# Performance work log

Measured on AMD Instinct MI355X. Metric: run time of the kernel, lower is better.

The kernel has to match this reference:

```python
import jax, jax.numpy as jnp
import numpy as np

D_MODEL = 1024
NHEAD = 16
D_K = D_MODEL // NHEAD


def setup_inputs() -> dict:
    key = jax.random.key(0)
    ks = jax.random.split(key, 12)
    B, L = 4, 2048
    s = 1.0 / np.sqrt(D_MODEL)
    inp = {
        "query": jax.random.normal(ks[0], (B, L, D_MODEL), jnp.float32),
        "key": jax.random.normal(ks[1], (B, L, D_MODEL), jnp.float32),
        "value": jax.random.normal(ks[2], (B, L, D_MODEL), jnp.float32),
        "Wq": jax.random.normal(ks[3], (D_MODEL, D_MODEL), jnp.float32) * s,
        "bq": jnp.zeros((D_MODEL,), jnp.float32),
        "Wk": jax.random.normal(ks[4], (D_MODEL, D_MODEL), jnp.float32) * s,
        "bk": jnp.zeros((D_MODEL,), jnp.float32),
        "Wv": jax.random.normal(ks[5], (D_MODEL, D_MODEL), jnp.float32) * s,
        "bv": jnp.zeros((D_MODEL,), jnp.float32),
        "Wo": jax.random.normal(ks[6], (D_MODEL, D_MODEL), jnp.float32) * s,
        "bo": jnp.zeros((D_MODEL,), jnp.float32),
    }
    return inp


def reference(query, key, value, Wq, bq, Wk, bk, Wv, bv, Wo, bo):
    B, Lq, _ = query.shape
    Lk = key.shape[1]
    # Linear projections, split into heads: [B, H, L, d_k]
    Q = (query @ Wq + bq).reshape(B, Lq, NHEAD, D_K).transpose(0, 2, 1, 3)
    K = (key @ Wk + bk).reshape(B, Lk, NHEAD, D_K).transpose(0, 2, 1, 3)
    V = (value @ Wv + bv).reshape(B, Lk, NHEAD, D_K).transpose(0, 2, 1, 3)
    scale = 1.0 / jnp.sqrt(jnp.asarray(D_K, Q.dtype))
    scores = jnp.einsum("bhqd,bhkd->bhqk", Q, K) * scale  # [B,H,Lq,Lk]
    attn = jax.nn.softmax(scores, axis=-1)
    context = jnp.einsum("bhqk,bhkd->bhqd", attn, V)
    context = context.transpose(0, 2, 1, 3).reshape(B, Lq, D_MODEL)
    return context @ Wo + bo
```

## Files before the change

kernel.cpp:

```cpp
#include <hip/hip_runtime.h>
#include <hip/hip_bf16.h>
#include <cstdint>
#include <cstddef>


typedef unsigned short u16;
typedef __bf16 bf8v __attribute__((ext_vector_type(8)));
typedef __bf16 bf4v __attribute__((ext_vector_type(4)));
typedef float f32x4 __attribute__((ext_vector_type(4)));

#define D_MODEL 1024
#define NHEAD   16
#define DK      64
#define BATCH   4
#define SEQ     2048
#define ROWS    (BATCH * SEQ)

__device__ __forceinline__ u16 f2b(float f) {
  union { float f; unsigned int i; } x; x.f = f;
  unsigned int r = x.i + 0x7fffu + ((x.i >> 16) & 1u);
  return (u16)(r >> 16);
}
__device__ __forceinline__ ushort4 pack4(float a, float b, float c, float d) {
  union { bf4v v; ushort4 u; } x;
  x.v[0] = (__bf16)a; x.v[1] = (__bf16)b; x.v[2] = (__bf16)c; x.v[3] = (__bf16)d;
  return x.u;
}
__device__ __forceinline__ void async16(const void* g, void* l) {
  __builtin_amdgcn_global_load_lds((const __attribute__((address_space(1))) void*)g,
                                   (__attribute__((address_space(3))) void*)l, 16, 0, 0);
}
#define MFMA16(a, b, c) __builtin_amdgcn_mfma_f32_16x16x32_bf16(a, b, c, 0, 0, 0)

__global__ void wtrans_cvt_kernel(const float* __restrict__ w0, const float* __restrict__ w1,
                                  const float* __restrict__ w2, const float* __restrict__ w3,
                                  u16* __restrict__ dst4) {
  __shared__ float t[32][33];
  const float* src = (blockIdx.z == 0) ? w0 : (blockIdx.z == 1) ? w1
                   : (blockIdx.z == 2) ? w2 : w3;
  u16* dst = dst4 + (size_t)blockIdx.z * D_MODEL * D_MODEL;
  const int c0 = blockIdx.x * 32, r0 = blockIdx.y * 32;
  for (int i = threadIdx.y; i < 32; i += 8)
    t[i][threadIdx.x] = src[(size_t)(r0 + i) * D_MODEL + c0 + threadIdx.x];
  __syncthreads();
  for (int i = threadIdx.y; i < 32; i += 8)
    dst[(size_t)(c0 + i) * D_MODEL + r0 + threadIdx.x] = f2b(t[threadIdx.x][i]);
}

__device__ __forceinline__ void gemm_epilogue(const f32x4 acc[4][4],
                                              const float* __restrict__ bias,
                                              void* __restrict__ out, int mode,
                                              float oscale, int m0, int n0,
                                              int wm, int wn, int quad, int l16) {
#pragma unroll
  for (int j = 0; j < 4; j++) {
    const int n = n0 + wn * 64 + j * 16 + l16;
    const float bv = bias[n];
#pragma unroll
    for (int i = 0; i < 4; i++) {
      const int gr0 = m0 + wm * 64 + i * 16 + quad * 4;
#pragma unroll
      for (int r = 0; r < 4; r++) {
        const int row = gr0 + r;
        const float val = (acc[i][j][r] + bv) * oscale;
        if (mode == 2) {
          ((float*)out)[(size_t)row * D_MODEL + n] = val;
        } else {
          const int b = row >> 11, l = row & 2047;
          const int h = n >> 6, d = n & 63;
          if (mode == 0)
            ((u16*)out)[(((size_t)(b * NHEAD + h) * SEQ + l) << 6) + d] = f2b(val);
          else
            ((u16*)out)[(((size_t)(b * NHEAD + h) * DK + d) << 11) + l] = f2b(val);
        }
      }
    }
  }
}

#define BM 128
#define BN 128
#define BK 32

__global__ __launch_bounds__(256) void gemm_qkv(const float* __restrict__ qa,
                                                const float* __restrict__ ka,
                                                const float* __restrict__ va,
                                                const u16* __restrict__ wt,
                                                const float* __restrict__ bq,
                                                const float* __restrict__ bk,
                                                const float* __restrict__ bv,
                                                u16* __restrict__ Qw, u16* __restrict__ Kw,
                                                u16* __restrict__ Vt, float qscale) {
  const int z = blockIdx.z;
  const float* A   = (z == 0) ? qa : (z == 1) ? ka : va;
  const u16* Bt    = wt + (size_t)z * D_MODEL * D_MODEL;
  const float* bia = (z == 0) ? bq : (z == 1) ? bk : bv;
  u16* out         = (z == 0) ? Qw : (z == 1) ? Kw : Vt;
  const int mode   = (z == 2) ? 1 : 0;
  const float osc  = (z == 0) ? qscale : 1.0f;

  __shared__ __align__(16) float Asf[BM * BK];
  __shared__ __align__(16) u16  Bs[BN * BK];
  const int tid = threadIdx.x;
  const int lane = tid & 63, wave = tid >> 6;
  const int wm = wave >> 1, wn = wave & 1;
  const int quad = lane >> 4, l16 = lane & 15;
  const int m0 = blockIdx.x * BM, n0 = blockIdx.y * BN;
  const int K = 1024;

  f32x4 acc[4][4];
#pragma unroll
  for (int i = 0; i < 4; i++)
#pragma unroll
    for (int j = 0; j < 4; j++) acc[i][j] = (f32x4){0.f, 0.f, 0.f, 0.f};

  const int arow = tid >> 3, achk = tid & 7;
  const int aswz = (achk ^ (arow & 7)) * 4;
  const float* Ag = A + (size_t)(m0 + arow) * K + aswz;
  const int brow = tid >> 2;
  const int bch = ((tid & 3) ^ ((tid >> 3) & 3)) * 8;
  const u16* Bg = Bt + (size_t)(n0 + brow) * K + bch;
  const int psw = l16 & 7;
  const int fsw = (quad ^ ((l16 >> 1) & 3)) * 8;

  for (int k0 = 0; k0 < K; k0 += BK) {
    async16(Ag + k0,                    &Asf[tid * 4]);
    async16(Ag + (size_t)32 * K + k0,   &Asf[1024 + tid * 4]);
    async16(Ag + (size_t)64 * K + k0,   &Asf[2048 + tid * 4]);
    async16(Ag + (size_t)96 * K + k0,   &Asf[3072 + tid * 4]);
    async16(Bg + k0,                    &Bs[tid * 8]);
    async16(Bg + (size_t)64 * K + k0,   &Bs[2048 + tid * 8]);
    __syncthreads();

    bf8v af[4], bfr[4];
#pragma unroll
    for (int i = 0; i < 4; i++) {
      const int row = wm * 64 + i * 16 + l16;
      const f32x4 a0 = *(const f32x4*)&Asf[row * 32 + ((quad * 2 + 0) ^ psw) * 4];
      const f32x4 a1 = *(const f32x4*)&Asf[row * 32 + ((quad * 2 + 1) ^ psw) * 4];
      bf8v t;
      t[0] = (__bf16)a0[0]; t[1] = (__bf16)a0[1]; t[2] = (__bf16)a0[2]; t[3] = (__bf16)a0[3];
      t[4] = (__bf16)a1[0]; t[5] = (__bf16)a1[1]; t[6] = (__bf16)a1[2]; t[7] = (__bf16)a1[3];
      af[i] = t;
    }
#pragma unroll
    for (int j = 0; j < 4; j++)
      bfr[j] = *(const bf8v*)&Bs[(wn * 64 + j * 16 + l16) * BK + fsw];
#pragma unroll
    for (int i = 0; i < 4; i++)
#pragma unroll
      for (int j = 0; j < 4; j++)
        acc[i][j] = MFMA16(af[i], bfr[j], acc[i][j]);
    __syncthreads();
  }
  gemm_epilogue(acc, bia, out, mode, osc, m0, n0, wm, wn, quad, l16);
}

__global__ __launch_bounds__(256) void gemm_bt(const u16* __restrict__ A,
                                               const u16* __restrict__ Bt,
                                               const float* __restrict__ bias,
                                               void* __restrict__ out, int mode,
                                               float oscale) {
  __shared__ __align__(16) u16 As[BM * BK];
  __shared__ __align__(16) u16 Bs[BN * BK];
  const int tid = threadIdx.x;
  const int lane = tid & 63, wave = tid >> 6;
  const int wm = wave >> 1, wn = wave & 1;
  const int quad = lane >> 4, l16 = lane & 15;
  const int m0 = blockIdx.x * BM, n0 = blockIdx.y * BN;
  const int K = 1024;

  f32x4 acc[4][4];
#pragma unroll
  for (int i = 0; i < 4; i++)
#pragma unroll
    for (int j = 0; j < 4; j++) acc[i][j] = (f32x4){0.f, 0.f, 0.f, 0.f};

  const int srow = tid >> 2;
  const int sch = ((tid & 3) ^ ((tid >> 3) & 3)) * 8;
  const int fsw = (quad ^ ((l16 >> 1) & 3)) * 8;
  const u16* Ag = A + (size_t)(m0 + srow) * K + sch;
  const u16* Bg = Bt + (size_t)(n0 + srow) * K + sch;

  for (int k0 = 0; k0 < K; k0 += BK) {
    async16(Ag + k0, &As[tid * 8]);
    async16(Ag + (size_t)64 * K + k0, &As[2048 + tid * 8]);
    async16(Bg + k0, &Bs[tid * 8]);
    async16(Bg + (size_t)64 * K + k0, &Bs[2048 + tid * 8]);
    __syncthreads();

    bf8v af[4], bfr[4];
#pragma unroll
    for (int i = 0; i < 4; i++)
      af[i] = *(const bf8v*)&As[(wm * 64 + i * 16 + l16) * BK + fsw];
#pragma unroll
    for (int j = 0; j < 4; j++)
      bfr[j] = *(const bf8v*)&Bs[(wn * 64 + j * 16 + l16) * BK + fsw];
#pragma unroll
    for (int i = 0; i < 4; i++)
#pragma unroll
      for (int j = 0; j < 4; j++)
        acc[i][j] = MFMA16(af[i], bfr[j], acc[i][j]);
    __syncthreads();
  }
  gemm_epilogue(acc, bias, out, mode, oscale, m0, n0, wm, wn, quad, l16);
}

__global__ __launch_bounds__(256, 3) void attn_kernel(const u16* __restrict__ Q,
                                                      const u16* __restrict__ K,
                                                      const u16* __restrict__ Vt,
                                                      u16* __restrict__ ctx) {
  const int bh = blockIdx.y;
  const int qb = blockIdx.x * 128;
  const int tid = threadIdx.x;
  const int lane = tid & 63, wave = tid >> 6;
  const int quad = lane >> 4, l16 = lane & 15;
  const u16* Qh = Q + (size_t)bh * SEQ * DK;
  const u16* Kh = K + (size_t)bh * SEQ * DK;
  const u16* Vh = Vt + (size_t)bh * DK * SEQ;

  __shared__ __align__(16) u16 Ks[2][2][64 * 32];
  __shared__ __align__(16) u16 Vs[2][2][64 * 32];
  __shared__ __align__(16) u16 Ps[4 * 32 * 72];

  const int srow = tid >> 2;
  const int sch  = ((tid & 3) ^ ((tid >> 3) & 3)) * 8;
  const int ldst = tid * 8;
  const int fsw  = (quad ^ ((l16 >> 1) & 3)) * 8;

  bf8v qf[2][2];
#pragma unroll
  for (int qg = 0; qg < 2; qg++)
#pragma unroll
    for (int h = 0; h < 2; h++)
      qf[qg][h] = *(const bf8v*)&Qh[(size_t)(qb + wave * 32 + qg * 16 + l16) * DK + h * 32 + quad * 8];

  f32x4 o[2][4];
  float m_q[2], l_q[2];
#pragma unroll
  for (int qg = 0; qg < 2; qg++) {
    m_q[qg] = -1e30f; l_q[qg] = 0.f;
#pragma unroll
    for (int d = 0; d < 4; d++) o[qg][d] = (f32x4){0.f, 0.f, 0.f, 0.f};
  }

  async16(Kh + (size_t)srow * DK + sch,       &Ks[0][0][ldst]);
  async16(Kh + (size_t)srow * DK + 32 + sch,  &Ks[0][1][ldst]);
  async16(Vh + (size_t)srow * SEQ + sch,      &Vs[0][0][ldst]);
  async16(Vh + (size_t)srow * SEQ + 32 + sch, &Vs[0][1][ldst]);
  __syncthreads();

  int p = 0;
  for (int kt = 0; kt < SEQ; kt += 64) {
    const int nt = kt + 64;
    if (nt < SEQ) {
      async16(Kh + (size_t)(nt + srow) * DK + sch,      &Ks[p ^ 1][0][ldst]);
      async16(Kh + (size_t)(nt + srow) * DK + 32 + sch, &Ks[p ^ 1][1][ldst]);
      async16(Vh + (size_t)srow * SEQ + nt + sch,       &Vs[p ^ 1][0][ldst]);
      async16(Vh + (size_t)srow * SEQ + nt + 32 + sch,  &Vs[p ^ 1][1][ldst]);
    }

    bf8v kf[4][2];
#pragma unroll
    for (int nb = 0; nb < 4; nb++)
#pragma unroll
      for (int h = 0; h < 2; h++)
        kf[nb][h] = *(const bf8v*)&Ks[p][h][(nb * 16 + l16) * 32 + fsw];

#pragma unroll
    for (int qg = 0; qg < 2; qg++) {
      f32x4 s[4];
#pragma unroll
      for (int nb = 0; nb < 4; nb++) {
        f32x4 t = (f32x4){0.f, 0.f, 0.f, 0.f};
        t = MFMA16(kf[nb][0], qf[qg][0], t);
        t = MFMA16(kf[nb][1], qf[qg][1], t);
        s[nb] = t;
      }
      float mx = s[0][0];
#pragma unroll
      for (int nb = 0; nb < 4; nb++)
#pragma unroll
        for (int r = 0; r < 4; r++) mx = fmaxf(mx, s[nb][r]);
      mx = fmaxf(mx, __shfl_xor(mx, 16));
      mx = fmaxf(mx, __shfl_xor(mx, 32));
      const float Mo = m_q[qg];
      const float Mn = fmaxf(Mo, mx);
      m_q[qg] = Mn;
      const float al = __builtin_amdgcn_exp2f(Mo - Mn);
      float rs = 0.f;
#pragma unroll
      for (int nb = 0; nb < 4; nb++)
#pragma unroll
        for (int r = 0; r < 4; r++) {
          const float pv = __builtin_amdgcn_exp2f(s[nb][r] - Mn);
          s[nb][r] = pv;
          rs += pv;
        }
      rs += __shfl_xor(rs, 16);
      rs += __shfl_xor(rs, 32);
      l_q[qg] = l_q[qg] * al + rs;
      if (__ballot(Mn > Mo)) {
#pragma unroll
        for (int d = 0; d < 4; d++) o[qg][d] *= al;
      }

      const int prow = (wave * 32 + qg * 16 + l16) * 72;
#pragma unroll
      for (int nb = 0; nb < 4; nb++)
        *(ushort4*)&Ps[prow + nb * 16 + quad * 4] =
            pack4(s[nb][0], s[nb][1], s[nb][2], s[nb][3]);
    }

    bf8v vf[4][2], pf[2][2];
#pragma unroll
    for (int dc = 0; dc < 4; dc++)
#pragma unroll
      for (int kc = 0; kc < 2; kc++)
        vf[dc][kc] = *(const bf8v*)&Vs[p][kc][(dc * 16 + l16) * 32 + fsw];
#pragma unroll
    for (int qg = 0; qg < 2; qg++)
#pragma unroll
      for (int kc = 0; kc < 2; kc++)
        pf[qg][kc] = *(const bf8v*)&Ps[(wave * 32 + qg * 16 + l16) * 72 + kc * 32 + quad * 8];
#pragma unroll
    for (int qg = 0; qg < 2; qg++)
#pragma unroll
      for (int dc = 0; dc < 4; dc++) {
        o[qg][dc] = MFMA16(vf[dc][0], pf[qg][0], o[qg][dc]);
        o[qg][dc] = MFMA16(vf[dc][1], pf[qg][1], o[qg][dc]);
      }

    __syncthreads();
    p ^= 1;
  }

  const int b = bh >> 4, hh = bh & 15;
#pragma unroll
  for (int qg = 0; qg < 2; qg++) {
    const float inv = __builtin_amdgcn_rcpf(l_q[qg]);
    const int q = qb + wave * 32 + qg * 16 + l16;
#pragma unroll
    for (int dc = 0; dc < 4; dc++) {
      const int col = hh * 64 + dc * 16 + quad * 4;
      *(ushort4*)&ctx[(size_t)(b * SEQ + q) * D_MODEL + col] =
          pack4(o[qg][dc][0] * inv, o[qg][dc][1] * inv,
                o[qg][dc][2] * inv, o[qg][dc][3] * inv);
    }
  }
}

extern "C" void kernel_launch(void* const* d_in, const int* in_sizes, int n_in,
                              void* d_out, int out_size, void* d_ws, size_t ws_size,
                              hipStream_t stream) {
  const float* q  = (const float*)d_in[0];
  const float* k  = (const float*)d_in[1];
  const float* v  = (const float*)d_in[2];
  const float* Wq = (const float*)d_in[3];
  const float* bq = (const float*)d_in[4];
  const float* Wk = (const float*)d_in[5];
  const float* bk = (const float*)d_in[6];
  const float* Wv = (const float*)d_in[7];
  const float* bv = (const float*)d_in[8];
  const float* Wo = (const float*)d_in[9];
  const float* bo = (const float*)d_in[10];

  u16* ws  = (u16*)d_ws;
  u16* wt  = ws;
  u16* ctx = wt + (size_t)4 * D_MODEL * D_MODEL;
  u16* Qw  = ctx + (size_t)ROWS * D_MODEL;
  u16* Kw  = Qw + (size_t)ROWS * D_MODEL;
  u16* Vt  = Kw + (size_t)ROWS * D_MODEL;

  const float QSCALE = 0.18033688011112042f;

  wtrans_cvt_kernel<<<dim3(32, 32, 4), dim3(32, 8), 0, stream>>>(Wq, Wk, Wv, Wo, wt);

  gemm_qkv<<<dim3(ROWS / BM, D_MODEL / BN, 3), 256, 0, stream>>>(
      q, k, v, wt, bq, bk, bv, Qw, Kw, Vt, QSCALE);

  attn_kernel<<<dim3(SEQ / 128, BATCH * NHEAD), 256, 0, stream>>>(Qw, Kw, Vt, ctx);

  gemm_bt<<<dim3(ROWS / BM, D_MODEL / BN), 256, 0, stream>>>(
      ctx, wt + (size_t)3 * D_MODEL * D_MODEL, bo, d_out, 2, 1.0f);
}
```

Baseline: 407.2 us.

## Double-buffer GEMM tiles with register prefetch and convert fp32 A before LDS

Replaces the single-buffered async-copy GEMM loops with a shared templated core. It prefetches the next K-tile into registers while MFMAs run on the current LDS buffer, then stores into a second buffer. For the QKV projection, fp32 activations are converted to bf16 in registers before the LDS store, which halves LDS footprint and read traffic. The trade-off is higher register pressure and a synchronous global-load path that loses the direct-to-LDS async copies.

After: 532.8 us. 30.8% more time.

```diff
diff --git a/kernel.cpp b/kernel.cpp
--- a/kernel.cpp
+++ b/kernel.cpp
@@ -82,6 +82,101 @@
 #define BN 128
 #define BK 32
 
+template<int AF32>
+__device__ __forceinline__ void gemm_core(const void* __restrict__ Aptr,
+                                          const u16* __restrict__ Bt,
+                                          const float* __restrict__ bias,
+                                          void* __restrict__ out, int mode,
+                                          float oscale) {
+  __shared__ __align__(16) u16 As[2][BM * BK];
+  __shared__ __align__(16) u16 Bs[2][BN * BK];
+  const int tid = threadIdx.x;
+  const int lane = tid & 63, wave = tid >> 6;
+  const int wm = wave >> 1, wn = wave & 1;
+  const int quad = lane >> 4, l16 = lane & 15;
+  const int m0 = blockIdx.x * BM, n0 = blockIdx.y * BN;
+  const int K = 1024;
+  const int srow = tid >> 2, sc = tid & 3;
+  const int wpos = (sc ^ ((srow >> 1) & 3)) * 8;
+  const int fsw  = (quad ^ ((l16 >> 1) & 3)) * 8;
+
+  const float* Af = (const float*)Aptr + (size_t)(m0 + srow) * K + sc * 8;
+  const u16*   Ah = (const u16*)Aptr + (size_t)(m0 + srow) * K + sc * 8;
+  const u16*   Bg = Bt + (size_t)(n0 + srow) * K + sc * 8;
+
+  f32x4 acc[4][4];
+#pragma unroll
+  for (int i = 0; i < 4; i++)
+#pragma unroll
+    for (int j = 0; j < 4; j++) acc[i][j] = (f32x4){0.f, 0.f, 0.f, 0.f};
+
+  float4 r0f[4], r1f[4];
+  uint4  r0h[2], r1h[2], r0b[2], r1b[2];
+
+  auto gload = [&](int k0, float4* rf, uint4* rh, uint4* rb) {
+    if (AF32) {
+      rf[0] = *(const float4*)(Af + k0);
+      rf[1] = *(const float4*)(Af + k0 + 4);
+      rf[2] = *(const float4*)(Af + (size_t)64 * K + k0);
+      rf[3] = *(const float4*)(Af + (size_t)64 * K + k0 + 4);
+    } else {
+      rh[0] = *(const uint4*)(Ah + k0);
+      rh[1] = *(const uint4*)(Ah + (size_t)64 * K + k0);
+    }
+    rb[0] = *(const uint4*)(Bg + k0);
+    rb[1] = *(const uint4*)(Bg + (size_t)64 * K + k0);
+  };
+  auto sstore = [&](int P, const float4* rf, const uint4* rh, const uint4* rb) {
+    if (AF32) {
+      bf8v t0, t1;
+#pragma unroll
+      for (int j = 0; j < 4; j++) {
+        t0[j] = (__bf16)rf[0][j]; t0[4 + j] = (__bf16)rf[1][j];
+        t1[j] = (__bf16)rf[2][j]; t1[4 + j] = (__bf16)rf[3][j];
+      }
+      *(bf8v*)&As[P][srow * 32 + wpos] = t0;
+      *(bf8v*)&As[P][(srow + 64) * 32 + wpos] = t1;
+    } else {
+      *(uint4*)&As[P][srow * 32 + wpos] = rh[0];
+      *(uint4*)&As[P][(srow + 64) * 32 + wpos] = rh[1];
+    }
+    *(uint4*)&Bs[P][srow * 32 + wpos] = rb[0];
+    *(uint4*)&Bs[P][(srow + 64) * 32 + wpos] = rb[1];
+  };
+  auto compute = [&](int P) {
+    bf8v af[4], bfr[4];
+#pragma unroll
+    for (int i = 0; i < 4; i++)
+      af[i] = *(const bf8v*)&As[P][(wm * 64 + i * 16 + l16) * 32 + fsw];
+#pragma unroll
+    for (int j = 0; j < 4; j++)
+      bfr[j] = *(const bf8v*)&Bs[P][(wn * 64 + j * 16 + l16) * 32 + fsw];
+#pragma unroll
+    for (int i = 0; i < 4; i++)
+#pragma unroll
+      for (int j = 0; j < 4; j++)
+        acc[i][j] = MFMA16(af[i], bfr[j], acc[i][j]);
+  };
+
+  gload(0, r0f, r0h, r0b);
+  sstore(0, r0f, r0h, r0b);
+  gload(32, r0f, r0h, r0b);
+  __syncthreads();
+
+  for (int it = 0; it < 16; it++) {
+    const int kc = it * 64;
+    gload(kc + 64 < K ? kc + 64 : K - 32, r1f, r1h, r1b);
+    compute(0);
+    sstore(1, r0f, r0h, r0b);
+    __syncthreads();
+    gload(kc + 96 < K ? kc + 96 : K - 32, r0f, r0h, r0b);
+    compute(1);
+    if (it < 15) sstore(0, r1f, r1h, r1b);
+    __syncthreads();
+  }
+  gemm_epilogue(acc, bias, out, mode, oscale, m0, n0, wm, wn, quad, l16);
+}
+
 __global__ __launch_bounds__(256) void gemm_qkv(const float* __restrict__ qa,
                                                 const float* __restrict__ ka,
                                                 const float* __restrict__ va,
@@ -92,118 +187,18 @@
                                                 u16* __restrict__ Qw, u16* __restrict__ Kw,
                                                 u16* __restrict__ Vt, float qscale) {
   const int z = blockIdx.z;
-  const float* A   = (z == 0) ? qa : (z == 1) ? ka : va;
+  const void* A    = (z == 0) ? (const void*)qa : (z == 1) ? (const void*)ka : (const void*)va;
   const u16* Bt    = wt + (size_t)z * D_MODEL * D_MODEL;
   const float* bia = (z == 0) ? bq : (z == 1) ? bk : bv;
-  u16* out         = (z == 0) ? Qw : (z == 1) ? Kw : Vt;
-  const int mode   = (z == 2) ? 1 : 0;
-  const float osc  = (z == 0) ? qscale : 1.0f;
-
-  __shared__ __align__(16) float Asf[BM * BK];
-  __shared__ __align__(16) u16  Bs[BN * BK];
-  const int tid = threadIdx.x;
-  const int lane = tid & 63, wave = tid >> 6;
-  const int wm = wave >> 1, wn = wave & 1;
-  const int quad = lane >> 4, l16 = lane & 15;
-  const int m0 = blockIdx.x * BM, n0 = blockIdx.y * BN;
-  const int K = 1024;
-
-  f32x4 acc[4][4];
-#pragma unroll
-  for (int i = 0; i < 4; i++)
-#pragma unroll
-    for (int j = 0; j < 4; j++) acc[i][j] = (f32x4){0.f, 0.f, 0.f, 0.f};
-
-  const int arow = tid >> 3, achk = tid & 7;
-  const int aswz = (achk ^ (arow & 7)) * 4;
-  const float* Ag = A + (size_t)(m0 + arow) * K + aswz;
-  const int brow = tid >> 2;
-  const int bch = ((tid & 3) ^ ((tid >> 3) & 3)) * 8;
-  const u16* Bg = Bt + (size_t)(n0 + brow) * K + bch;
-  const int psw = l16 & 7;
-  const int fsw = (quad ^ ((l16 >> 1) & 3)) * 8;
-
-  for (int k0 = 0; k0 < K; k0 += BK) {
-    async16(Ag + k0,                    &Asf[tid * 4]);
-    async16(Ag + (size_t)32 * K + k0,   &Asf[1024 + tid * 4]);
-    async16(Ag + (size_t)64 * K + k0,   &Asf[2048 + tid * 4]);
-    async16(Ag + (size_t)96 * K + k0,   &Asf[3072 + tid * 4]);
-    async16(Bg + k0,                    &Bs[tid * 8]);
-    async16(Bg + (size_t)64 * K + k0,   &Bs[2048 + tid * 8]);
-    __syncthreads();
-
-    bf8v af[4], bfr[4];
-#pragma unroll
-    for (int i = 0; i < 4; i++) {
-      const int row = wm * 64 + i * 16 + l16;
-      const f32x4 a0 = *(const f32x4*)&Asf[row * 32 + ((quad * 2 + 0) ^ psw) * 4];
-      const f32x4 a1 = *(const f32x4*)&Asf[row * 32 + ((quad * 2 + 1) ^ psw) * 4];
-      bf8v t;
-      t[0] = (__bf16)a0[0]; t[1] = (__bf16)a0[1]; t[2] = (__bf16)a0[2]; t[3] = (__bf16)a0[3];
-      t[4] = (__bf16)a1[0]; t[5] = (__bf16)a1[1]; t[6] = (__bf16)a1[2]; t[7] = (__bf16)a1[3];
-      af[i] = t;
-    }
-#pragma unroll
-    for (int j = 0; j < 4; j++)
-      bfr[j] = *(const bf8v*)&Bs[(wn * 64 + j * 16 + l16) * BK + fsw];
-#pragma unroll
-    for (int i = 0; i < 4; i++)
-#pragma unroll
-      for (int j = 0; j < 4; j++)
-        acc[i][j] = MFMA16(af[i], bfr[j], acc[i][j]);
-    __syncthreads();
-  }
-  gemm_epilogue(acc, bia, out, mode, osc, m0, n0, wm, wn, quad, l16);
-}
-
-__global__ __launch_bounds__(256) void gemm_bt(const u16* __restrict__ A,
-                                               const u16* __restrict__ Bt,
-                                               const float* __restrict__ bias,
-                                               void* __restrict__ out, int mode,
-                                               float oscale) {
-  __shared__ __align__(16) u16 As[BM * BK];
-  __shared__ __align__(16) u16 Bs[BN * BK];
-  const int tid = threadIdx.x;
-  const int lane = tid & 63, wave = tid >> 6;
-  const int wm = wave >> 1, wn = wave & 1;
-  const int quad = lane >> 4, l16 = lane & 15;
-  const int m0 = blockIdx.x * BM, n0 = blockIdx.y * BN;
-  const int K = 1024;
-
-  f32x4 acc[4][4];
-#pragma unroll
-  for (int i = 0; i < 4; i++)
-#pragma unroll
-    for (int j = 0; j < 4; j++) acc[i][j] = (f32x4){0.f, 0.f, 0.f, 0.f};
-
-  const int srow = tid >> 2;
-  const int sch = ((tid & 3) ^ ((tid >> 3) & 3)) * 8;
-  const int fsw = (quad ^ ((l16 >> 1) & 3)) * 8;
-  const u16* Ag = A + (size_t)(m0 + srow) * K + sch;
-  const u16* Bg = Bt + (size_t)(n0 + srow) * K + sch;
-
-  for (int k0 = 0; k0 < K; k0 += BK) {
-    async16(Ag + k0, &As[tid * 8]);
-    async16(Ag + (size_t)64 * K + k0, &As[2048 + tid * 8]);
-    async16(Bg + k0, &Bs[tid * 8]);
-    async16(Bg + (size_t)64 * K + k0, &Bs[2048 + tid * 8]);
-    __syncthreads();
-
-    bf8v af[4], bfr[4];
-#pragma unroll
-    for (int i = 0; i < 4; i++)
-      af[i] = *(const bf8v*)&As[(wm * 64 + i * 16 + l16) * BK + fsw];
-#pragma unroll
-    for (int j = 0; j < 4; j++)
-      bfr[j] = *(const bf8v*)&Bs[(wn * 64 + j * 16 + l16) * BK + fsw];
-#pragma unroll
-    for (int i = 0; i < 4; i++)
-#pragma unroll
-      for (int j = 0; j < 4; j++)
-        acc[i][j] = MFMA16(af[i], bfr[j], acc[i][j]);
-    __syncthreads();
-  }
-  gemm_epilogue(acc, bias, out, mode, oscale, m0, n0, wm, wn, quad, l16);
+  void* out        = (z == 0) ? (void*)Qw : (z == 1) ? (void*)Kw : (void*)Vt;
+  gemm_core<1>(A, Bt, bia, out, (z == 2) ? 1 : 0, (z == 0) ? qscale : 1.0f);
+}
+
+__global__ __launch_bounds__(256) void gemm_out(const u16* __restrict__ A,
+                                                const u16* __restrict__ Bt,
+                                                const float* __restrict__ bias,
+                                                float* __restrict__ out) {
+  gemm_core<0>(A, Bt, bias, out, 2, 1.0f);
 }
 
 __global__ __launch_bounds__(256, 3) void attn_kernel(const u16* __restrict__ Q,
@@ -381,6 +376,6 @@
 
   attn_kernel<<<dim3(SEQ / 128, BATCH * NHEAD), 256, 0, stream>>>(Qw, Kw, Vt, ctx);
 
-  gemm_bt<<<dim3(ROWS / BM, D_MODEL / BN), 256, 0, stream>>>(
-      ctx, wt + (size_t)3 * D_MODEL * D_MODEL, bo, d_out, 2, 1.0f);
-}
+  gemm_out<<<dim3(ROWS / BM, D_MODEL / BN), 256, 0, stream>>>(
+      ctx, wt + (size_t)3 * D_MODEL * D_MODEL, bo, (float*)d_out);
+}
```

## Double-buffer GEMM tiles with register prefetch and convert A to bf16 before LDS

Applied to the files above, without the earlier changes.

Both projection GEMMs move from synchronous async-copy loads with two barriers per K-step to a register-prefetched, double-buffered LDS pipeline. Global loads for the next two K-slices are issued while MFMAs run on the current buffer. In the QKV GEMM the fp32 activations are now converted to bf16 in registers before the LDS store, which halves A-tile LDS footprint and bandwidth. The cost is more live registers, which may reduce occupancy, and a somewhat awkward clamped prefetch at the tail.

Result: slower. 422.5 us (+3.7%).

```diff
diff --git a/kernel.cpp b/kernel.cpp
--- a/kernel.cpp
+++ b/kernel.cpp
@@ -80,7 +80,51 @@
 
 #define BM 128
 #define BN 128
-#define BK 32
+#define GK 1024
+
+__device__ __forceinline__ void ld_a32(const float* p, int k0,
+                                       float4& x0, float4& x1, float4& x2, float4& x3) {
+  x0 = *(const float4*)(p + k0);
+  x1 = *(const float4*)(p + k0 + 4);
+  x2 = *(const float4*)(p + (size_t)64 * GK + k0);
+  x3 = *(const float4*)(p + (size_t)64 * GK + k0 + 4);
+}
+__device__ __forceinline__ void ld_h16(const u16* p, int k0, uint4& x0, uint4& x1) {
+  x0 = *(const uint4*)(p + k0);
+  x1 = *(const uint4*)(p + (size_t)64 * GK + k0);
+}
+__device__ __forceinline__ void st_a32(u16* dst, int srow, int wpos,
+                                       const float4& x0, const float4& x1,
+                                       const float4& x2, const float4& x3) {
+  bf8v t0, t1;
+#pragma unroll
+  for (int j = 0; j < 4; j++) {
+    t0[j] = (__bf16)x0[j]; t0[4 + j] = (__bf16)x1[j];
+    t1[j] = (__bf16)x2[j]; t1[4 + j] = (__bf16)x3[j];
+  }
+  *(bf8v*)&dst[srow * 32 + wpos] = t0;
+  *(bf8v*)&dst[(srow + 64) * 32 + wpos] = t1;
+}
+__device__ __forceinline__ void st_h16(u16* dst, int srow, int wpos,
+                                       const uint4& x0, const uint4& x1) {
+  *(uint4*)&dst[srow * 32 + wpos] = x0;
+  *(uint4*)&dst[(srow + 64) * 32 + wpos] = x1;
+}
+__device__ __forceinline__ void tile_mfma(const u16* As, const u16* Bs, f32x4 acc[4][4],
+                                          int wm, int wn, int quad, int l16, int fsw) {
+  bf8v af[4], bfr[4];
+#pragma unroll
+  for (int i = 0; i < 4; i++)
+    af[i] = *(const bf8v*)&As[(wm * 64 + i * 16 + l16) * 32 + fsw];
+#pragma unroll
+  for (int j = 0; j < 4; j++)
+    bfr[j] = *(const bf8v*)&Bs[(wn * 64 + j * 16 + l16) * 32 + fsw];
+#pragma unroll
+  for (int i = 0; i < 4; i++)
+#pragma unroll
+    for (int j = 0; j < 4; j++)
+      acc[i][j] = MFMA16(af[i], bfr[j], acc[i][j]);
+}
 
 __global__ __launch_bounds__(256) void gemm_qkv(const float* __restrict__ qa,
                                                 const float* __restrict__ ka,
@@ -95,18 +139,23 @@
   const float* A   = (z == 0) ? qa : (z == 1) ? ka : va;
   const u16* Bt    = wt + (size_t)z * D_MODEL * D_MODEL;
   const float* bia = (z == 0) ? bq : (z == 1) ? bk : bv;
-  u16* out         = (z == 0) ? Qw : (z == 1) ? Kw : Vt;
+  void* out        = (z == 0) ? (void*)Qw : (z == 1) ? (void*)Kw : (void*)Vt;
   const int mode   = (z == 2) ? 1 : 0;
   const float osc  = (z == 0) ? qscale : 1.0f;
 
-  __shared__ __align__(16) float Asf[BM * BK];
-  __shared__ __align__(16) u16  Bs[BN * BK];
+  __shared__ __align__(16) u16 As[2][BM * 32];
+  __shared__ __align__(16) u16 Bs[2][BN * 32];
   const int tid = threadIdx.x;
   const int lane = tid & 63, wave = tid >> 6;
   const int wm = wave >> 1, wn = wave & 1;
   const int quad = lane >> 4, l16 = lane & 15;
   const int m0 = blockIdx.x * BM, n0 = blockIdx.y * BN;
-  const int K = 1024;
+  const int srow = tid >> 2, sc = tid & 3;
+  const int wpos = (sc ^ ((srow >> 1) & 3)) * 8;
+  const int fsw  = (quad ^ ((l16 >> 1) & 3)) * 8;
+
+  const float* Ag = A + (size_t)(m0 + srow) * GK + sc * 8;
+  const u16*   Bg = Bt + (size_t)(n0 + srow) * GK + sc * 8;
 
   f32x4 acc[4][4];
 #pragma unroll
@@ -114,61 +163,50 @@
 #pragma unroll
     for (int j = 0; j < 4; j++) acc[i][j] = (f32x4){0.f, 0.f, 0.f, 0.f};
 
-  const int arow = tid >> 3, achk = tid & 7;
-  const int aswz = (achk ^ (arow & 7)) * 4;
-  const float* Ag = A + (size_t)(m0 + arow) * K + aswz;
-  const int brow = tid >> 2;
-  const int bch = ((tid & 3) ^ ((tid >> 3) & 3)) * 8;
-  const u16* Bg = Bt + (size_t)(n0 + brow) * K + bch;
-  const int psw = l16 & 7;
-  const int fsw = (quad ^ ((l16 >> 1) & 3)) * 8;
-
-  for (int k0 = 0; k0 < K; k0 += BK) {
-    async16(Ag + k0,                    &Asf[tid * 4]);
-    async16(Ag + (size_t)32 * K + k0,   &Asf[1024 + tid * 4]);
-    async16(Ag + (size_t)64 * K + k0,   &Asf[2048 + tid * 4]);
-    async16(Ag + (size_t)96 * K + k0,   &Asf[3072 + tid * 4]);
-    async16(Bg + k0,                    &Bs[tid * 8]);
-    async16(Bg + (size_t)64 * K + k0,   &Bs[2048 + tid * 8]);
+  float4 f00, f01, f02, f03, f10, f11, f12, f13;
+  uint4  b00, b01, b10, b11;
+
+  ld_a32(Ag, 0, f00, f01, f02, f03);  ld_h16(Bg, 0, b00, b01);
+  st_a32(As[0], srow, wpos, f00, f01, f02, f03);  st_h16(Bs[0], srow, wpos, b00, b01);
+  ld_a32(Ag, 32, f10, f11, f12, f13); ld_h16(Bg, 32, b10, b11);
+  __syncthreads();
+
+  for (int it = 0; it < 16; it++) {
+    int ke = it * 64 + 64; if (ke > GK - 32) ke = GK - 32;
+    int ko = it * 64 + 96; if (ko > GK - 32) ko = GK - 32;
+    ld_a32(Ag, ke, f00, f01, f02, f03);  ld_h16(Bg, ke, b00, b01);
+    tile_mfma(As[0], Bs[0], acc, wm, wn, quad, l16, fsw);
+    st_a32(As[1], srow, wpos, f10, f11, f12, f13);
+    st_h16(Bs[1], srow, wpos, b10, b11);
     __syncthreads();
-
-    bf8v af[4], bfr[4];
-#pragma unroll
-    for (int i = 0; i < 4; i++) {
-      const int row = wm * 64 + i * 16 + l16;
-      const f32x4 a0 = *(const f32x4*)&Asf[row * 32 + ((quad * 2 + 0) ^ psw) * 4];
-      const f32x4 a1 = *(const f32x4*)&Asf[row * 32 + ((quad * 2 + 1) ^ psw) * 4];
-      bf8v t;
-      t[0] = (__bf16)a0[0]; t[1] = (__bf16)a0[1]; t[2] = (__bf16)a0[2]; t[3] = (__bf16)a0[3];
-      t[4] = (__bf16)a1[0]; t[5] = (__bf16)a1[1]; t[6] = (__bf16)a1[2]; t[7] = (__bf16)a1[3];
-      af[i] = t;
-    }
-#pragma unroll
-    for (int j = 0; j < 4; j++)
-      bfr[j] = *(const bf8v*)&Bs[(wn * 64 + j * 16 + l16) * BK + fsw];
-#pragma unroll
-    for (int i = 0; i < 4; i++)
-#pragma unroll
-      for (int j = 0; j < 4; j++)
-        acc[i][j] = MFMA16(af[i], bfr[j], acc[i][j]);
+    ld_a32(Ag, ko, f10, f11, f12, f13);  ld_h16(Bg, ko, b10, b11);
+    tile_mfma(As[1], Bs[1], acc, wm, wn, quad, l16, fsw);
+    if (it < 15) {
+      st_a32(As[0], srow, wpos, f00, f01, f02, f03);
+      st_h16(Bs[0], srow, wpos, b00, b01);
+    }
     __syncthreads();
   }
   gemm_epilogue(acc, bia, out, mode, osc, m0, n0, wm, wn, quad, l16);
 }
 
-__global__ __launch_bounds__(256) void gemm_bt(const u16* __restrict__ A,
-                                               const u16* __restrict__ Bt,
-                                               const float* __restrict__ bias,
-                                               void* __restrict__ out, int mode,
-                                               float oscale) {
-  __shared__ __align__(16) u16 As[BM * BK];
-  __shared__ __align__(16) u16 Bs[BN * BK];
+__global__ __launch_bounds__(256) void gemm_out(const u16* __restrict__ A,
+                                                const u16* __restrict__ Bt,
+                                                const float* __restrict__ bias,
+                                                float* __restrict__ out) {
+  __shared__ __align__(16) u16 As[2][BM * 32];
+  __shared__ __align__(16) u16 Bs[2][BN * 32];
   const int tid = threadIdx.x;
   const int lane = tid & 63, wave = tid >> 6;
   const int wm = wave >> 1, wn = wave & 1;
   const int quad = lane >> 4, l16 = lane & 15;
   const int m0 = blockIdx.x * BM, n0 = blockIdx.y * BN;
-  const int K = 1024;
+  const int srow = tid >> 2, sc = tid & 3;
+  const int wpos = (sc ^ ((srow >> 1) & 3)) * 8;
+  const int fsw  = (quad ^ ((l16 >> 1) & 3)) * 8;
+
+  const u16* Ag = A + (size_t)(m0 + srow) * GK + sc * 8;
+  const u16* Bg = Bt + (size_t)(n0 + srow) * GK + sc * 8;
 
   f32x4 acc[4][4];
 #pragma unroll
@@ -176,34 +214,28 @@
 #pragma unroll
     for (int j = 0; j < 4; j++) acc[i][j] = (f32x4){0.f, 0.f, 0.f, 0.f};
 
-  const int srow = tid >> 2;
-  const int sch = ((tid & 3) ^ ((tid >> 3) & 3)) * 8;
-  const int fsw = (quad ^ ((l16 >> 1) & 3)) * 8;
-  const u16* Ag = A + (size_t)(m0 + srow) * K + sch;
-  const u16* Bg = Bt + (size_t)(n0 + srow) * K + sch;
-
-  for (int k0 = 0; k0 < K; k0 += BK) {
-    async16(Ag + k0, &As[tid * 8]);
-    async16(Ag + (size_t)64 * K + k0, &As[2048 + tid * 8]);
-    async16(Bg + k0, &Bs[tid * 8]);
-    async16(Bg + (size_t)64 * K + k0, &Bs[2048 + tid * 8]);
+  uint4 a00, a01, a10, a11, b00, b01, b10, b11;
+
+  ld_h16(Ag, 0, a00, a01);  ld_h16(Bg, 0, b00, b01);
+  st_h16(As[0], srow, wpos, a00, a01);  st_h16(Bs[0], srow, wpos, b00, b01);
+  ld_h16(Ag, 32, a10, a11); ld_h16(Bg, 32, b10, b11);
+  __syncthreads();
+
+  for (int it = 0; it < 16; it++) {
+    int ke = it * 64 + 64; if (ke > GK - 32) ke = GK - 32;
+    int ko = it * 64 + 96; if (ko > GK - 32) ko = GK - 32;
+    ld_h16(Ag, ke, a00, a01);  ld_h16(Bg, ke, b00, b01);
+    tile_mfma(As[0], Bs[0], acc, wm, wn, quad, l16, fsw);
+    st_h16(As[1], srow, wpos, a10, a11);  st_h16(Bs[1], srow, wpos, b10, b11);
     __syncthreads();
-
-    bf8v af[4], bfr[4];
-#pragma unroll
-    for (int i = 0; i < 4; i++)
-      af[i] = *(const bf8v*)&As[(wm * 64 + i * 16 + l16) * BK + fsw];
-#pragma unroll
-    for (int j = 0; j < 4; j++)
-      bfr[j] = *(const bf8v*)&Bs[(wn * 64 + j * 16 + l16) * BK + fsw];
-#pragma unroll
-    for (int i = 0; i < 4; i++)
-#pragma unroll
-      for (int j = 0; j < 4; j++)
-        acc[i][j] = MFMA16(af[i], bfr[j], acc[i][j]);
+    ld_h16(Ag, ko, a10, a11);  ld_h16(Bg, ko, b10, b11);
+    tile_mfma(As[1], Bs[1], acc, wm, wn, quad, l16, fsw);
+    if (it < 15) {
+      st_h16(As[0], srow, wpos, a00, a01);  st_h16(Bs[0], srow, wpos, b00, b01);
+    }
     __syncthreads();
   }
-  gemm_epilogue(acc, bias, out, mode, oscale, m0, n0, wm, wn, quad, l16);
+  gemm_epilogue(acc, bias, out, 2, 1.0f, m0, n0, wm, wn, quad, l16);
 }
 
 __global__ __launch_bounds__(256, 3) void attn_kernel(const u16* __restrict__ Q,
@@ -381,6 +413,6 @@
 
   attn_kernel<<<dim3(SEQ / 128, BATCH * NHEAD), 256, 0, stream>>>(Qw, Kw, Vt, ctx);
 
-  gemm_bt<<<dim3(ROWS / BM, D_MODEL / BN), 256, 0, stream>>>(
-      ctx, wt + (size_t)3 * D_MODEL * D_MODEL, bo, d_out, 2, 1.0f);
-}
+  gemm_out<<<dim3(ROWS / BM, D_MODEL / BN), 256, 0, stream>>>(
+      ctx, wt + (size_t)3 * D_MODEL * D_MODEL, bo, (float*)d_out);
+}
```
